# Optimization experiments

Hardware: AMD Instinct MI355X
Metric: run time of the kernel (lower is better)

The kernel has to match this reference:

```python
import jax, jax.numpy as jnp
import numpy as np

VOXEL_OFFSETS = jnp.array([-3.0, -3.0, -1.0], dtype=jnp.float32)
VOXEL_SIZE = 0.05


def setup_inputs() -> dict:
    key = jax.random.key(0)
    k1, k2 = jax.random.split(key)
    B, N = 4, 4096
    preds = jax.random.normal(k1, (B, N, 3), dtype=jnp.float32)
    gts = jax.random.normal(k2, (B, N, 3), dtype=jnp.float32)
    return {"preds": preds, "gts": gts}


def _chamfer(x, y):
    # x: [B, Nx, 3], y: [B, Ny, 3]
    # squared pairwise distances P[b, i, j] = ||x_bi - y_bj||^2
    xx = jnp.sum(x * x, axis=-1)  # [B, Nx]
    yy = jnp.sum(y * y, axis=-1)  # [B, Ny]
    zz = jnp.einsum('bnd,bmd->bnm', x, y)  # [B, Nx, Ny]
    P = xx[:, :, None] + yy[:, None, :] - 2.0 * zz
    dist1 = jnp.min(P, axis=2)  # nearest gt for each pred point, [B, Nx]
    dist2 = jnp.min(P, axis=1)  # nearest pred for each gt point, [B, Ny]
    return jnp.mean(dist1) + jnp.mean(dist2)


def _voxelize2(coord):
    # torch.div(coord - offsets, 0.05, rounding_mode='trunc') -> float grid coords
    return jnp.trunc((coord - VOXEL_OFFSETS) / VOXEL_SIZE)


def reference(preds, gts):
    # loss2 (point-space chamfer) is computed in the original but only logged
    loss2 = _chamfer(preds, gts)
    gts_voxel = _voxelize2(gts.astype(jnp.float32))
    preds_voxel = _voxelize2(preds.astype(jnp.float32))
    loss1 = _chamfer(preds_voxel, gts_voxel)
    # original forward returns loss1 only
    return loss1
```

## Files before the change

### kernel.cpp

```cpp
#include <hip/hip_runtime.h>
#include <math.h>


typedef float  f32x16 __attribute__((ext_vector_type(16)));
typedef short  bf16x8 __attribute__((ext_vector_type(8)));

constexpr int NPTS   = 4096;
constexpr int BLK    = 1024;
constexpr int QPB    = 128;
constexpr int NTB    = NPTS / QPB;
constexpr int BATCH  = 4;
constexpr int NBLOCKS = 2 * BATCH * NTB;
constexpr int CHUNK  = 2048;
constexpr float FINF  = 3.402823466e38f;
constexpr float SCALE = 1.0f / 16384.0f;

__device__ __forceinline__ float vox(float c, float off) {
    return truncf((c + off) * 20.0f);
}
__device__ __forceinline__ unsigned cvtpk(float lo, float hi) {
    unsigned r;
    asm("v_cvt_pk_bf16_f32 %0, %1, %2" : "=v"(r) : "v"(lo), "v"(hi));
    return r;
}
__device__ __forceinline__ float min3f(float a, float b, float c) {
    return fminf(fminf(a, b), c);
}
__device__ __forceinline__ int4 packB(float x, float y, float z) {
    const float yy = fmaf(z, z, fmaf(y, y, x * x));
    const float hi = floorf(yy * 0.00390625f) * 256.0f;
    const float lo = yy - hi;
    return make_int4((int)cvtpk(x, y),
                     (int)cvtpk(z, hi),
                     (int)cvtpk(lo, 0.0f),
                     0);
}

__global__ __launch_bounds__(BLK, 4) void chamfer_rows_kernel(
    const float* __restrict__ preds,
    const float* __restrict__ gts,
    float* __restrict__ partials)
{
    __shared__ int4  cfrag[CHUNK];
    __shared__ int4  qfrag[QPB];
    __shared__ float qxx[QPB];
    __shared__ float waveRow[16][32];

    const int t    = threadIdx.x;
    const int bid  = blockIdx.x;
    const int dir  = bid >> 7;
    const int rem  = bid & 127;
    const int b    = rem >> 5;
    const int tile = rem & 31;
    const int w    = t >> 6;
    const int g    = w >> 2;
    const int wsub = w & 3;
    const int lane = t & 63;
    const int col  = lane & 31;
    const bool lo_g = (lane < 32);

    const float* __restrict__ xb = (dir ? gts : preds) + (size_t)b * NPTS * 3;
    const float* __restrict__ yb = (dir ? preds : gts) + (size_t)b * NPTS * 3;

    if (t < QPB) {
        const int qi = tile * QPB + t;
        const float x = vox(xb[qi*3+0], 3.0f);
        const float y = vox(xb[qi*3+1], 3.0f);
        const float z = vox(xb[qi*3+2], 1.0f);
        qxx[t] = fmaf(z, z, fmaf(y, y, x * x));
        const float mx = -2.0f * x, my = -2.0f * y, mz = -2.0f * z;
        qfrag[t] = make_int4((int)cvtpk(mx, my),
                             (int)cvtpk(mz, 1.0f),
                             (int)cvtpk(1.0f, 0.0f),
                             0);
    }
    __syncthreads();

    bf16x8 afrag;
    {
        const int4 qv = qfrag[g * 32 + col];
        int4 ai = { lo_g ? qv.x : 0, lo_g ? qv.y : 0, lo_g ? qv.z : 0, 0 };
        afrag = __builtin_bit_cast(bf16x8, ai);
    }

    f32x16 rm;
    #pragma unroll
    for (int i = 0; i < 16; ++i) rm[i] = FINF;
    const f32x16 zero = {};

    const float2* __restrict__ yb2 = (const float2*)yb;

    #pragma unroll 1
    for (int cc = 0; cc < 2; ++cc) {
        if (cc) __syncthreads();
        {
            const int p0 = t * 2;
            const int fi = cc * 3072 + t * 3;
            const float2 r0 = yb2[fi + 0];
            const float2 r1 = yb2[fi + 1];
            const float2 r2 = yb2[fi + 2];
            cfrag[p0+0] = packB(vox(r0.x,3.f), vox(r0.y,3.f), vox(r1.x,1.f));
            cfrag[p0+1] = packB(vox(r1.y,3.f), vox(r2.x,3.f), vox(r2.y,1.f));
        }
        __syncthreads();

        const int4* __restrict__ bbase = &cfrag[wsub * 512 + col];
        #pragma unroll
        for (int jp = 0; jp < 8; ++jp) {
            const bf16x8 bfa = __builtin_bit_cast(bf16x8, bbase[jp * 64]);
            const bf16x8 bfb = __builtin_bit_cast(bf16x8, bbase[jp * 64 + 32]);
            const f32x16 dA = __builtin_amdgcn_mfma_f32_32x32x16_bf16(
                afrag, bfa, zero, 0, 0, 0);
            const f32x16 dB = __builtin_amdgcn_mfma_f32_32x32x16_bf16(
                afrag, bfb, zero, 0, 0, 0);
            #pragma unroll
            for (int i = 0; i < 16; ++i)
                rm[i] = min3f(rm[i], dA[i], dB[i]);
        }
    }

    const int hi4 = (lane >> 5) * 4;
    #pragma unroll
    for (int i = 0; i < 16; ++i) {
        float v = rm[i];
        v = fminf(v, __shfl_xor(v, 1, 64));
        v = fminf(v, __shfl_xor(v, 2, 64));
        v = fminf(v, __shfl_xor(v, 4, 64));
        v = fminf(v, __shfl_xor(v, 8, 64));
        v = fminf(v, __shfl_xor(v, 16, 64));
        const int r = (i & 3) + 8 * (i >> 2) + hi4;
        if (col == 0) waveRow[w][r] = v + qxx[g * 32 + r];
    }
    __syncthreads();

    if ((w & 3) == 0) {
        float s = 0.0f;
        if (lane < 32) {
            s = fminf(fminf(waveRow[w + 0][lane], waveRow[w + 1][lane]),
                      fminf(waveRow[w + 2][lane], waveRow[w + 3][lane]));
        }
        #pragma unroll
        for (int o = 32; o >= 1; o >>= 1) s += __shfl_xor(s, o, 64);
        if (lane == 0) partials[bid * 4 + g] = s;
    }
}

__global__ __launch_bounds__(256) void chamfer_finish_kernel(
    const float* __restrict__ partials, float* __restrict__ out)
{
    __shared__ float s1[256];
    const int t = threadIdx.x;
    s1[t] = (partials[t] + partials[t + 256])
          + (partials[t + 512] + partials[t + 768]);
    __syncthreads();
    for (int k = 128; k > 0; k >>= 1) {
        if (t < k) s1[t] += s1[t + k];
        __syncthreads();
    }
    if (t == 0) out[0] = s1[0] * SCALE;
}

extern "C" void kernel_launch(void* const* d_in, const int* in_sizes, int n_in,
                              void* d_out, int out_size, void* d_ws, size_t ws_size,
                              hipStream_t stream)
{
    const float* preds = (const float*)d_in[0];
    const float* gts   = (const float*)d_in[1];
    float* out = (float*)d_out;
    float* partials = (float*)d_ws;

    chamfer_rows_kernel<<<NBLOCKS, BLK, 0, stream>>>(preds, gts, partials);
    chamfer_finish_kernel<<<1, 256, 0, stream>>>(partials, out);
}
```

Measured before the change: 16.82 us.

## Give each wave two query fragments to reuse candidate LDS loads

Each wave now holds two 32-query A fragments and processes 256 candidates instead of four waves sharing 32 queries over 512 candidates. Each B fragment read from LDS feeds two MFMAs, halving LDS traffic per MFMA, and the cross-wave reduction now combines eight waves per 64 queries. The cost is more accumulator registers per wave, which may pressure occupancy under the launch bounds, and the partials layout shrinks to two per block.

```diff
diff --git a/kernel.cpp b/kernel.cpp
--- a/kernel.cpp
+++ b/kernel.cpp
@@ -44,7 +44,7 @@
     __shared__ int4  cfrag[CHUNK];
     __shared__ int4  qfrag[QPB];
     __shared__ float qxx[QPB];
-    __shared__ float waveRow[16][32];
+    __shared__ float waveRow[16][64];
 
     const int t    = threadIdx.x;
     const int bid  = blockIdx.x;
@@ -53,8 +53,8 @@
     const int b    = rem >> 5;
     const int tile = rem & 31;
     const int w    = t >> 6;
-    const int g    = w >> 2;
-    const int wsub = w & 3;
+    const int tp   = w >> 3;
+    const int s    = w & 7;
     const int lane = t & 63;
     const int col  = lane & 31;
     const bool lo_g = (lane < 32);
@@ -76,16 +76,19 @@
     }
     __syncthreads();
 
-    bf16x8 afrag;
+    bf16x8 afrag0, afrag1;
     {
-        const int4 qv = qfrag[g * 32 + col];
-        int4 ai = { lo_g ? qv.x : 0, lo_g ? qv.y : 0, lo_g ? qv.z : 0, 0 };
-        afrag = __builtin_bit_cast(bf16x8, ai);
+        const int4 q0 = qfrag[tp * 64 + col];
+        const int4 q1 = qfrag[tp * 64 + 32 + col];
+        int4 a0 = { lo_g ? q0.x : 0, lo_g ? q0.y : 0, lo_g ? q0.z : 0, 0 };
+        int4 a1 = { lo_g ? q1.x : 0, lo_g ? q1.y : 0, lo_g ? q1.z : 0, 0 };
+        afrag0 = __builtin_bit_cast(bf16x8, a0);
+        afrag1 = __builtin_bit_cast(bf16x8, a1);
     }
 
-    f32x16 rm;
+    f32x16 rm0, rm1;
     #pragma unroll
-    for (int i = 0; i < 16; ++i) rm[i] = FINF;
+    for (int i = 0; i < 16; ++i) { rm0[i] = FINF; rm1[i] = FINF; }
     const f32x16 zero = {};
 
     const float2* __restrict__ yb2 = (const float2*)yb;
@@ -104,44 +107,59 @@
         }
         __syncthreads();
 
-        const int4* __restrict__ bbase = &cfrag[wsub * 512 + col];
+        const int4* __restrict__ bbase = &cfrag[s * 256 + col];
         #pragma unroll
-        for (int jp = 0; jp < 8; ++jp) {
+        for (int jp = 0; jp < 4; ++jp) {
             const bf16x8 bfa = __builtin_bit_cast(bf16x8, bbase[jp * 64]);
             const bf16x8 bfb = __builtin_bit_cast(bf16x8, bbase[jp * 64 + 32]);
-            const f32x16 dA = __builtin_amdgcn_mfma_f32_32x32x16_bf16(
-                afrag, bfa, zero, 0, 0, 0);
-            const f32x16 dB = __builtin_amdgcn_mfma_f32_32x32x16_bf16(
-                afrag, bfb, zero, 0, 0, 0);
+            const f32x16 d0a = __builtin_amdgcn_mfma_f32_32x32x16_bf16(
+                afrag0, bfa, zero, 0, 0, 0);
+            const f32x16 d0b = __builtin_amdgcn_mfma_f32_32x32x16_bf16(
+                afrag0, bfb, zero, 0, 0, 0);
+            const f32x16 d1a = __builtin_amdgcn_mfma_f32_32x32x16_bf16(
+                afrag1, bfa, zero, 0, 0, 0);
+            const f32x16 d1b = __builtin_amdgcn_mfma_f32_32x32x16_bf16(
+                afrag1, bfb, zero, 0, 0, 0);
             #pragma unroll
-            for (int i = 0; i < 16; ++i)
-                rm[i] = min3f(rm[i], dA[i], dB[i]);
+            for (int i = 0; i < 16; ++i) {
+                rm0[i] = min3f(rm0[i], d0a[i], d0b[i]);
+                rm1[i] = min3f(rm1[i], d1a[i], d1b[i]);
+            }
         }
     }
 
     const int hi4 = (lane >> 5) * 4;
     #pragma unroll
     for (int i = 0; i < 16; ++i) {
-        float v = rm[i];
-        v = fminf(v, __shfl_xor(v, 1, 64));
-        v = fminf(v, __shfl_xor(v, 2, 64));
-        v = fminf(v, __shfl_xor(v, 4, 64));
-        v = fminf(v, __shfl_xor(v, 8, 64));
-        v = fminf(v, __shfl_xor(v, 16, 64));
+        float v0 = rm0[i], v1 = rm1[i];
+        v0 = fminf(v0, __shfl_xor(v0, 1, 64));
+        v1 = fminf(v1, __shfl_xor(v1, 1, 64));
+        v0 = fminf(v0, __shfl_xor(v0, 2, 64));
+        v1 = fminf(v1, __shfl_xor(v1, 2, 64));
+        v0 = fminf(v0, __shfl_xor(v0, 4, 64));
+        v1 = fminf(v1, __shfl_xor(v1, 4, 64));
+        v0 = fminf(v0, __shfl_xor(v0, 8, 64));
+        v1 = fminf(v1, __shfl_xor(v1, 8, 64));
+        v0 = fminf(v0, __shfl_xor(v0, 16, 64));
+        v1 = fminf(v1, __shfl_xor(v1, 16, 64));
         const int r = (i & 3) + 8 * (i >> 2) + hi4;
-        if (col == 0) waveRow[w][r] = v + qxx[g * 32 + r];
+        if (col == 0) {
+            waveRow[w][r]      = v0;
+            waveRow[w][32 + r] = v1;
+        }
     }
     __syncthreads();
 
-    if ((w & 3) == 0) {
-        float s = 0.0f;
-        if (lane < 32) {
-            s = fminf(fminf(waveRow[w + 0][lane], waveRow[w + 1][lane]),
-                      fminf(waveRow[w + 2][lane], waveRow[w + 3][lane]));
-        }
+    if (s == 0) {
+        const int wbase = tp * 8;
+        float m = waveRow[wbase][lane];
         #pragma unroll
-        for (int o = 32; o >= 1; o >>= 1) s += __shfl_xor(s, o, 64);
-        if (lane == 0) partials[bid * 4 + g] = s;
+        for (int k = 1; k < 8; ++k)
+            m = fminf(m, waveRow[wbase + k][lane]);
+        float v = m + qxx[tp * 64 + lane];
+        #pragma unroll
+        for (int o = 32; o >= 1; o >>= 1) v += __shfl_xor(v, o, 64);
+        if (lane == 0) partials[bid * 2 + tp] = v;
     }
 }
 
@@ -150,8 +168,7 @@
 {
     __shared__ float s1[256];
     const int t = threadIdx.x;
-    s1[t] = (partials[t] + partials[t + 256])
-          + (partials[t + 512] + partials[t + 768]);
+    s1[t] = partials[t] + partials[t + 256];
     __syncthreads();
     for (int k = 128; k > 0; k >>= 1) {
         if (t < k) s1[t] += s1[t + k];
```

Measured after the change: 19.92 us. 18.5% more time.
